# Kernel optimization log

Measured on AMD Instinct MI355X. Metric: run time of the kernel, lower is better.

The kernel has to match this reference:

```python
import jax, jax.numpy as jnp
import numpy as np

B, S, D_IN, D_H = 8, 2048, 512, 512

def setup_inputs() -> dict:
    key = jax.random.key(0)
    ks = jax.random.split(key, 7)
    scale = 1.0 / np.sqrt(D_IN)
    return {
        "x": jax.random.normal(ks[0], (B, S, D_IN), dtype=jnp.float32),
        "Wq": jax.random.uniform(ks[1], (D_IN, D_H), jnp.float32, -scale, scale),
        "bq": jax.random.uniform(ks[2], (D_H,), jnp.float32, -scale, scale),
        "Wk": jax.random.uniform(ks[3], (D_IN, D_H), jnp.float32, -scale, scale),
        "bk": jax.random.uniform(ks[4], (D_H,), jnp.float32, -scale, scale),
        "Wv": jax.random.uniform(ks[5], (D_IN, D_H), jnp.float32, -scale, scale),
        "bv": jax.random.uniform(ks[6], (D_H,), jnp.float32, -scale, scale),
    }

def reference(x, Wq, bq, Wk, bk, Wv, bv):
    q = jnp.einsum("bsd,dh->bsh", x, Wq) + bq  # [B,S,H]
    k = jnp.einsum("bsd,dh->bsh", x, Wk) + bk
    v = jnp.einsum("bsd,dh->bsh", x, Wv) + bv
    # NOTE: original has NO 1/sqrt(d) scaling — faithful reproduction
    scores = jnp.einsum("bqh,bkh->bqk", q, k)  # [B,S,S]
    probs = jax.nn.softmax(scores, axis=-1)
    return jnp.einsum("bqk,bkh->bqh", probs, v)
```

## Files before the change

### kernel.cpp

```cpp
#include <hip/hip_runtime.h>


typedef __attribute__((ext_vector_type(8))) _Float16 f16x8;
typedef __attribute__((ext_vector_type(8))) short bf16x8;
typedef __attribute__((ext_vector_type(4))) float f32x4;

__device__ __forceinline__ unsigned short f2h(float f) {
  _Float16 h = (_Float16)f;
  return *(unsigned short*)&h;
}
__device__ __forceinline__ unsigned short f2bf(float f) {
  unsigned int u = __float_as_uint(f);
  unsigned int r = (u + 0x7fffu + ((u >> 16) & 1u)) >> 16;
  return (unsigned short)r;
}
__device__ __forceinline__ float bf2f(unsigned short h) {
  return __uint_as_float(((unsigned int)h) << 16);
}

__device__ __forceinline__ void load_lds16(const void* g, void* l) {
  __builtin_amdgcn_global_load_lds(
      (const __attribute__((address_space(1))) unsigned int*)g,
      (__attribute__((address_space(3))) unsigned int*)l, 16, 0, 0);
}

__global__ __launch_bounds__(256) void convx_kernel(const float* __restrict__ x,
                                                    unsigned short* __restrict__ xh) {
  int i = blockIdx.x * 256 + threadIdx.x;
  float4 v = ((const float4*)x)[i];
  union { unsigned short h[4]; short4 s4; } u;
  u.h[0] = f2h(v.x); u.h[1] = f2h(v.y); u.h[2] = f2h(v.z); u.h[3] = f2h(v.w);
  ((short4*)xh)[i] = u.s4;
}

__global__ __launch_bounds__(256) void convw_kernel(
    const float* __restrict__ W0, const float* __restrict__ W1,
    const float* __restrict__ W2, unsigned short* __restrict__ Wt) {
  const float* W = (blockIdx.z == 0) ? W0 : (blockIdx.z == 1) ? W1 : W2;
  unsigned short* t = Wt + (size_t)blockIdx.z * 512 * 512;
  __shared__ float tile[32][33];
  int tx = threadIdx.x, ty = threadIdx.y;
  int h0 = blockIdx.x * 32, d0 = blockIdx.y * 32;
  for (int i = ty; i < 32; i += 8) tile[i][tx] = W[(long)(d0 + i) * 512 + h0 + tx];
  __syncthreads();
  for (int i = ty; i < 32; i += 8)
    t[(long)(h0 + i) * 512 + d0 + tx] = f2h(tile[tx][i]);
}

__global__ __launch_bounds__(256) void gemm_qkv_kernel(
    const unsigned short* __restrict__ A,
    const unsigned short* __restrict__ Bt,
    unsigned short* __restrict__ Qo, unsigned short* __restrict__ Ko,
    unsigned short* __restrict__ VTo,
    const float* __restrict__ bq, const float* __restrict__ bk,
    const float* __restrict__ bv) {
  __shared__ alignas(16) unsigned short As[128 * 32];
  __shared__ alignas(16) unsigned short Bs[128 * 32];
  const int t = threadIdx.x;
  const long long bm = (long long)blockIdx.x * 128;
  const long long bn = (long long)blockIdx.y * 128;

  const int ar = t >> 2;
  const int ac = (t & 3) * 8;

  f32x4 acc[4][4];
#pragma unroll
  for (int i = 0; i < 4; i++)
#pragma unroll
    for (int j = 0; j < 4; j++) acc[i][j] = {0.f, 0.f, 0.f, 0.f};

  const int lane = t & 63;
  const int wave = t >> 6;
  const int wm = (wave & 1) * 64;
  const int wn = (wave >> 1) * 64;
  const int fm = lane & 15;
  const int k8 = (lane >> 4) * 8;

  for (int kt = 0; kt < 512; kt += 32) {
#pragma unroll
    for (int r = 0; r < 2; r++)
      load_lds16(A + (bm + r * 64 + ar) * 512 + kt + ac, &As[r * 2048 + t * 8]);
#pragma unroll
    for (int r = 0; r < 2; r++)
      load_lds16(Bt + (bn + r * 64 + ar) * 512 + kt + ac, &Bs[r * 2048 + t * 8]);
    __syncthreads();

    f16x8 af[4], bfr[4];
#pragma unroll
    for (int i = 0; i < 4; i++)
      af[i] = *(const f16x8*)&As[(wm + i * 16 + fm) * 32 + k8];
#pragma unroll
    for (int j = 0; j < 4; j++)
      bfr[j] = *(const f16x8*)&Bs[(wn + j * 16 + fm) * 32 + k8];
#pragma unroll
    for (int i = 0; i < 4; i++)
#pragma unroll
      for (int j = 0; j < 4; j++)
        acc[i][j] = __builtin_amdgcn_mfma_f32_16x16x32_f16(af[i], bfr[j], acc[i][j], 0, 0, 0);
    __syncthreads();
  }

  const int crow = (lane >> 4) * 4;
  const int ccol = lane & 15;
#pragma unroll
  for (int j = 0; j < 4; j++) {
    const long long col = bn + wn + j * 16 + ccol;
    float bias = (col < 512) ? bq[col] : (col < 1024) ? bk[col - 512] : bv[col - 1024];
#pragma unroll
    for (int i = 0; i < 4; i++) {
      const long long row0 = bm + wm + i * 16 + crow;
      if (col >= 1024) {
        const long long b = row0 >> 11;
        const long long s = row0 & 2047;
        const long long dcol = col - 1024;
        union { unsigned short h[4]; short4 s4; } u;
#pragma unroll
        for (int r = 0; r < 4; r++) u.h[r] = f2bf(acc[i][j][r] + bias);
        *(short4*)(VTo + (((b * 64 + (s >> 5)) * 512 + dcol) * 32 + (s & 31))) = u.s4;
      } else {
        unsigned short* dst = (col < 512) ? (Qo + row0 * 512 + col)
                                          : (Ko + row0 * 512 + (col - 512));
#pragma unroll
        for (int r = 0; r < 4; r++) dst[(size_t)r * 512] = f2h(acc[i][j][r] + bias);
      }
    }
  }
}

__global__ __launch_bounds__(512, 2) void attn_fused_kernel(
    const unsigned short* __restrict__ Qg,
    const unsigned short* __restrict__ Kg,
    const unsigned short* __restrict__ Vt,
    float* __restrict__ out) {
  __shared__ alignas(16) unsigned short SB[2][16384];
  __shared__ alignas(16) unsigned short Qh[16384];
  __shared__ alignas(16) unsigned short Ps[8192];
  __shared__ float rsw[4][64];

  const int t = threadIdx.x;
  const int lane = t & 63;
  const int w = t >> 6;
  const int fm = lane & 15;
  const int g = lane >> 4;
  const int qh = w & 1;
  const int kg = w >> 1;
  const int b = blockIdx.x & 7;
  const int q0 = (blockIdx.x >> 3) << 6;

  const unsigned short* Qb = Qg + ((size_t)b * 2048 + q0) * 512;
  const unsigned short* Kb = Kg + (size_t)b * 2048 * 512;
  const unsigned short* Vb = Vt + (size_t)b * 2048 * 512;

  int ksrc[4], qsrc[4]; unsigned int sdst[4];
#pragma unroll
  for (int r = 0; r < 4; ++r) {
    const int L = r * 8192 + t * 16;
    sdst[r] = L >> 1;
    const int kr = L >> 8;
    ksrc[r] = kr * 512 + (((L & 255) ^ ((kr & 7) << 4)) >> 1);
    const int qr = L >> 9;
    qsrc[r] = qr * 512 + (((L & 511) ^ ((qr & 7) << 4)) >> 1);
  }

#pragma unroll
  for (int r = 0; r < 4; ++r) load_lds16(Qb + qsrc[r], &SB[0][sdst[r]]);
#pragma unroll
  for (int r = 0; r < 4; ++r) load_lds16(Qb + 256 + qsrc[r], &Qh[sdst[r]]);
  asm volatile("s_waitcnt vmcnt(4)" ::: "memory");
  __builtin_amdgcn_s_barrier();

  const int swz = (fm & 7) << 4;
  f16x8 qf[2][8];
#pragma unroll
  for (int j = 0; j < 2; ++j)
#pragma unroll
    for (int ds = 0; ds < 8; ++ds)
      qf[j][ds] = *(const f16x8*)((const char*)SB[0] +
          (qh * 32 + j * 16 + fm) * 512 + ((g * 16 + ds * 64) ^ swz));
  asm volatile("s_waitcnt lgkmcnt(0)" ::: "memory");
  __builtin_amdgcn_s_barrier();
#pragma unroll
  for (int r = 0; r < 4; ++r) load_lds16(Kb + ksrc[r], &SB[0][sdst[r]]);

  f32x4 oacc[2][8];
#pragma unroll
  for (int i = 0; i < 2; ++i)
#pragma unroll
    for (int jj = 0; jj < 8; ++jj) oacc[i][jj] = {0.f, 0.f, 0.f, 0.f};
  float psum0 = 0.f, psum1 = 0.f;
  f32x4 sacc[2][2];

  for (int kt = 0; kt < 16; ++kt) {
    const size_t kbase = (size_t)kt * 65536;
#pragma unroll
    for (int u = 0; u < 8; ++u) {
      unsigned short* cur = SB[u & 1];
      unsigned short* nxt = SB[(u & 1) ^ 1];
      if (u < 3) {
#pragma unroll
        for (int r = 0; r < 4; ++r)
          load_lds16(Kb + kbase + (u + 1) * 128 + ksrc[r], &nxt[sdst[r]]);
      } else if (u < 7) {
        const unsigned short* vs = Vb + (size_t)(kt * 4 + (u - 3)) * 16384;
#pragma unroll
        for (int r = 0; r < 4; ++r) load_lds16(vs + sdst[r], &nxt[sdst[r]]);
      } else if (kt < 15) {
#pragma unroll
        for (int r = 0; r < 4; ++r)
          load_lds16(Kb + kbase + 65536 + ksrc[r], &nxt[sdst[r]]);
      }
      if (kt == 15 && u == 7)
        asm volatile("s_waitcnt vmcnt(0)" ::: "memory");
      else
        asm volatile("s_waitcnt vmcnt(4)" ::: "memory");
      __builtin_amdgcn_s_barrier();
      __builtin_amdgcn_sched_barrier(0);

      __builtin_amdgcn_s_setprio(1);
      if (u < 4) {
        if (u == 0) {
          sacc[0][0] = {0.f, 0.f, 0.f, 0.f}; sacc[0][1] = {0.f, 0.f, 0.f, 0.f};
          sacc[1][0] = {0.f, 0.f, 0.f, 0.f}; sacc[1][1] = {0.f, 0.f, 0.f, 0.f};
        }
#pragma unroll
        for (int s = 0; s < 4; ++s) {
          const f16x8 a0 = *(const f16x8*)((const char*)cur +
              (kg * 32 + fm) * 256 + ((g * 16 + s * 64) ^ swz));
          const f16x8 a1 = *(const f16x8*)((const char*)cur +
              (kg * 32 + 16 + fm) * 256 + ((g * 16 + s * 64) ^ swz));
          f16x8 b0, b1;
          if (u < 2) {
            b0 = qf[0][u * 4 + s]; b1 = qf[1][u * 4 + s];
          } else {
            const int dz = (g * 16 + ((u - 2) * 4 + s) * 64) ^ swz;
            b0 = *(const f16x8*)((const char*)Qh + (qh * 32 + fm) * 512 + dz);
            b1 = *(const f16x8*)((const char*)Qh + (qh * 32 + 16 + fm) * 512 + dz);
          }
          sacc[0][0] = __builtin_amdgcn_mfma_f32_16x16x32_f16(a0, b0, sacc[0][0], 0, 0, 0);
          sacc[0][1] = __builtin_amdgcn_mfma_f32_16x16x32_f16(a0, b1, sacc[0][1], 0, 0, 0);
          sacc[1][0] = __builtin_amdgcn_mfma_f32_16x16x32_f16(a1, b0, sacc[1][0], 0, 0, 0);
          sacc[1][1] = __builtin_amdgcn_mfma_f32_16x16x32_f16(a1, b1, sacc[1][1], 0, 0, 0);
        }
        if (u == 3) {
#pragma unroll
          for (int i = 0; i < 2; ++i)
#pragma unroll
            for (int j = 0; j < 2; ++j) {
              const int q = qh * 32 + j * 16 + fm;
              const int k2 = (kg * 32 + i * 16 + g * 4) * 2;
              union { unsigned short h[4]; short4 s4; } uu;
              float s0 = 0.f;
#pragma unroll
              for (int r = 0; r < 4; ++r) {
                const unsigned short pb = f2bf(__expf(sacc[i][j][r]));
                uu.h[r] = pb; s0 += bf2f(pb);
              }
              if (j == 0) psum0 += s0; else psum1 += s0;
              *(short4*)((char*)Ps + q * 256 + (k2 ^ swz)) = uu.s4;
            }
        }
      } else {
        const int ju = u - 4;
        const bf16x8 p0 = *(const bf16x8*)((const char*)Ps +
            (qh * 32 + fm) * 256 + ((ju * 64 + g * 16) ^ swz));
        const bf16x8 p1 = *(const bf16x8*)((const char*)Ps +
            (qh * 32 + 16 + fm) * 256 + ((ju * 64 + g * 16) ^ swz));
#pragma unroll
        for (int jj = 0; jj < 8; ++jj) {
          const bf16x8 vf = *(const bf16x8*)((const char*)cur +
              (kg * 128 + jj * 16 + fm) * 64 + g * 16);
          oacc[0][jj] = __builtin_amdgcn_mfma_f32_16x16x32_bf16(p0, vf, oacc[0][jj], 0, 0, 0);
          oacc[1][jj] = __builtin_amdgcn_mfma_f32_16x16x32_bf16(p1, vf, oacc[1][jj], 0, 0, 0);
        }
      }
      __builtin_amdgcn_s_setprio(0);
      asm volatile("s_waitcnt lgkmcnt(0)" ::: "memory");
      __builtin_amdgcn_s_barrier();
    }
  }

  psum0 += __shfl_xor(psum0, 16); psum0 += __shfl_xor(psum0, 32);
  psum1 += __shfl_xor(psum1, 16); psum1 += __shfl_xor(psum1, 32);
  if (g == 0) {
    rsw[kg][qh * 32 + fm] = psum0;
    rsw[kg][qh * 32 + 16 + fm] = psum1;
  }
  __syncthreads();

  float* ob = out + ((size_t)b * 2048 + q0) * 512;
#pragma unroll
  for (int i = 0; i < 2; ++i) {
    float inv[4];
#pragma unroll
    for (int r = 0; r < 4; ++r) {
      const int q = qh * 32 + i * 16 + g * 4 + r;
      inv[r] = 1.0f / (rsw[0][q] + rsw[1][q] + rsw[2][q] + rsw[3][q]);
    }
#pragma unroll
    for (int jj = 0; jj < 8; ++jj) {
      const int d = kg * 128 + jj * 16 + fm;
#pragma unroll
      for (int r = 0; r < 4; ++r)
        ob[(size_t)(qh * 32 + i * 16 + g * 4 + r) * 512 + d] = oacc[i][jj][r] * inv[r];
    }
  }
}

extern "C" void kernel_launch(void* const* d_in, const int* in_sizes, int n_in,
                              void* d_out, int out_size, void* d_ws, size_t ws_size,
                              hipStream_t stream) {
  const float* x  = (const float*)d_in[0];
  const float* Wq = (const float*)d_in[1];
  const float* bq = (const float*)d_in[2];
  const float* Wk = (const float*)d_in[3];
  const float* bk = (const float*)d_in[4];
  const float* Wv = (const float*)d_in[5];
  const float* bv = (const float*)d_in[6];
  float* out = (float*)d_out;

  const size_t SZ = (size_t)16384 * 512 * 2;
  char* p = (char*)d_ws;
  unsigned short* xh = (unsigned short*)p; p += SZ;
  unsigned short* Wt = (unsigned short*)p; p += (size_t)3 * 512 * 512 * 2;
  unsigned short* Qb = (unsigned short*)p; p += SZ;
  unsigned short* Kb = (unsigned short*)p; p += SZ;
  unsigned short* VT = (unsigned short*)p; p += SZ;

  convx_kernel<<<8192, 256, 0, stream>>>(x, xh);
  convw_kernel<<<dim3(16, 16, 3), dim3(32, 8), 0, stream>>>(Wq, Wk, Wv, Wt);
  gemm_qkv_kernel<<<dim3(128, 12), 256, 0, stream>>>(xh, Wt, Qb, Kb, VT, bq, bk, bv);
  attn_fused_kernel<<<256, 512, 0, stream>>>(Qb, Kb, VT, out);
}
```

Before: 246.6 us.

## Use four-slot LDS ring with two-stage prefetch and keep full Q in registers

After: 301.2 us. 22.1% more time.

```diff
diff --git a/kernel.cpp b/kernel.cpp
--- a/kernel.cpp
+++ b/kernel.cpp
@@ -132,8 +132,7 @@
     const unsigned short* __restrict__ Kg,
     const unsigned short* __restrict__ Vt,
     float* __restrict__ out) {
-  __shared__ alignas(16) unsigned short SB[2][16384];
-  __shared__ alignas(16) unsigned short Qh[16384];
+  __shared__ alignas(16) unsigned short SB[4][16384];
   __shared__ alignas(16) unsigned short Ps[8192];
   __shared__ float rsw[4][64];
 
@@ -158,29 +157,35 @@
     sdst[r] = L >> 1;
     const int kr = L >> 8;
     ksrc[r] = kr * 512 + (((L & 255) ^ ((kr & 7) << 4)) >> 1);
-    const int qr = L >> 9;
-    qsrc[r] = qr * 512 + (((L & 511) ^ ((qr & 7) << 4)) >> 1);
+    const int qr = L >> 10;
+    qsrc[r] = qr * 512 + (((L & 1023) ^ ((qr & 7) << 4)) >> 1);
   }
 
 #pragma unroll
   for (int r = 0; r < 4; ++r) load_lds16(Qb + qsrc[r], &SB[0][sdst[r]]);
 #pragma unroll
-  for (int r = 0; r < 4; ++r) load_lds16(Qb + 256 + qsrc[r], &Qh[sdst[r]]);
-  asm volatile("s_waitcnt vmcnt(4)" ::: "memory");
+  for (int r = 0; r < 4; ++r) load_lds16(Qb + 32 * 512 + qsrc[r], &SB[1][sdst[r]]);
+  asm volatile("s_waitcnt vmcnt(0)" ::: "memory");
   __builtin_amdgcn_s_barrier();
+  __builtin_amdgcn_sched_barrier(0);
 
   const int swz = (fm & 7) << 4;
-  f16x8 qf[2][8];
-#pragma unroll
-  for (int j = 0; j < 2; ++j)
-#pragma unroll
-    for (int ds = 0; ds < 8; ++ds)
-      qf[j][ds] = *(const f16x8*)((const char*)SB[0] +
-          (qh * 32 + j * 16 + fm) * 512 + ((g * 16 + ds * 64) ^ swz));
+  f16x8 qf[2][16];
+#pragma unroll
+  for (int j = 0; j < 2; ++j) {
+    const char* qbase = (const char*)SB[qh] + (j * 16 + fm) * 1024;
+#pragma unroll
+    for (int ds = 0; ds < 16; ++ds)
+      qf[j][ds] = *(const f16x8*)(qbase + ((ds * 64 + g * 16) ^ swz));
+  }
   asm volatile("s_waitcnt lgkmcnt(0)" ::: "memory");
   __builtin_amdgcn_s_barrier();
+  __builtin_amdgcn_sched_barrier(0);
+
 #pragma unroll
   for (int r = 0; r < 4; ++r) load_lds16(Kb + ksrc[r], &SB[0][sdst[r]]);
+#pragma unroll
+  for (int r = 0; r < 4; ++r) load_lds16(Kb + 128 + ksrc[r], &SB[1][sdst[r]]);
 
   f32x4 oacc[2][8];
 #pragma unroll
@@ -194,53 +199,61 @@
     const size_t kbase = (size_t)kt * 65536;
 #pragma unroll
     for (int u = 0; u < 8; ++u) {
-      unsigned short* cur = SB[u & 1];
-      unsigned short* nxt = SB[(u & 1) ^ 1];
-      if (u < 3) {
+      unsigned short* nxt = SB[(u + 2) & 3];
+      if (u == 0) {
 #pragma unroll
         for (int r = 0; r < 4; ++r)
-          load_lds16(Kb + kbase + (u + 1) * 128 + ksrc[r], &nxt[sdst[r]]);
-      } else if (u < 7) {
-        const unsigned short* vs = Vb + (size_t)(kt * 4 + (u - 3)) * 16384;
+          load_lds16(Kb + kbase + 2 * 128 + ksrc[r], &nxt[sdst[r]]);
+      } else if (u == 1) {
+#pragma unroll
+        for (int r = 0; r < 4; ++r)
+          load_lds16(Kb + kbase + 3 * 128 + ksrc[r], &nxt[sdst[r]]);
+      } else if (u < 6) {
+        const unsigned short* vs = Vb + (size_t)(kt * 4 + (u - 2)) * 16384;
 #pragma unroll
         for (int r = 0; r < 4; ++r) load_lds16(vs + sdst[r], &nxt[sdst[r]]);
-      } else if (kt < 15) {
-#pragma unroll
-        for (int r = 0; r < 4; ++r)
-          load_lds16(Kb + kbase + 65536 + ksrc[r], &nxt[sdst[r]]);
+      } else if (u == 6) {
+        if (kt < 15) {
+#pragma unroll
+          for (int r = 0; r < 4; ++r)
+            load_lds16(Kb + kbase + 65536 + ksrc[r], &nxt[sdst[r]]);
+        }
+      } else {
+        if (kt < 15) {
+#pragma unroll
+          for (int r = 0; r < 4; ++r)
+            load_lds16(Kb + kbase + 65536 + 128 + ksrc[r], &nxt[sdst[r]]);
+        }
       }
-      if (kt == 15 && u == 7)
-        asm volatile("s_waitcnt vmcnt(0)" ::: "memory");
-      else
-        asm volatile("s_waitcnt vmcnt(4)" ::: "memory");
+      if (u >= 6 && kt == 15) {
+        if (u == 6) asm volatile("s_waitcnt vmcnt(4)" ::: "memory");
+        else        asm volatile("s_waitcnt vmcnt(0)" ::: "memory");
+      } else {
+        asm volatile("s_waitcnt vmcnt(8)" ::: "memory");
+      }
       __builtin_amdgcn_s_barrier();
       __builtin_amdgcn_sched_barrier(0);
 
-      __builtin_amdgcn_s_setprio(1);
+      const unsigned short* cur = SB[u & 3];
       if (u < 4) {
         if (u == 0) {
           sacc[0][0] = {0.f, 0.f, 0.f, 0.f}; sacc[0][1] = {0.f, 0.f, 0.f, 0.f};
           sacc[1][0] = {0.f, 0.f, 0.f, 0.f}; sacc[1][1] = {0.f, 0.f, 0.f, 0.f};
         }
+        __builtin_amdgcn_s_setprio(1);
 #pragma unroll
         for (int s = 0; s < 4; ++s) {
-          const f16x8 a0 = *(const f16x8*)((const char*)cur +
-              (kg * 32 + fm) * 256 + ((g * 16 + s * 64) ^ swz));
-          const f16x8 a1 = *(const f16x8*)((const char*)cur +
-              (kg * 32 + 16 + fm) * 256 + ((g * 16 + s * 64) ^ swz));
-          f16x8 b0, b1;
-          if (u < 2) {
-            b0 = qf[0][u * 4 + s]; b1 = qf[1][u * 4 + s];
-          } else {
-            const int dz = (g * 16 + ((u - 2) * 4 + s) * 64) ^ swz;
-            b0 = *(const f16x8*)((const char*)Qh + (qh * 32 + fm) * 512 + dz);
-            b1 = *(const f16x8*)((const char*)Qh + (qh * 32 + 16 + fm) * 512 + dz);
-          }
+          const int off = (s * 64 + g * 16) ^ swz;
+          const f16x8 a0 = *(const f16x8*)((const char*)cur + (kg * 32 + fm) * 256 + off);
+          const f16x8 a1 = *(const f16x8*)((const char*)cur + (kg * 32 + 16 + fm) * 256 + off);
+          const f16x8 b0 = qf[0][u * 4 + s];
+          const f16x8 b1 = qf[1][u * 4 + s];
           sacc[0][0] = __builtin_amdgcn_mfma_f32_16x16x32_f16(a0, b0, sacc[0][0], 0, 0, 0);
           sacc[0][1] = __builtin_amdgcn_mfma_f32_16x16x32_f16(a0, b1, sacc[0][1], 0, 0, 0);
           sacc[1][0] = __builtin_amdgcn_mfma_f32_16x16x32_f16(a1, b0, sacc[1][0], 0, 0, 0);
           sacc[1][1] = __builtin_amdgcn_mfma_f32_16x16x32_f16(a1, b1, sacc[1][1], 0, 0, 0);
         }
+        __builtin_amdgcn_s_setprio(0);
         if (u == 3) {
 #pragma unroll
           for (int i = 0; i < 2; ++i)
@@ -258,6 +271,7 @@
               if (j == 0) psum0 += s0; else psum1 += s0;
               *(short4*)((char*)Ps + q * 256 + (k2 ^ swz)) = uu.s4;
             }
+          asm volatile("s_waitcnt lgkmcnt(0)" ::: "memory");
         }
       } else {
         const int ju = u - 4;
@@ -265,6 +279,7 @@
             (qh * 32 + fm) * 256 + ((ju * 64 + g * 16) ^ swz));
         const bf16x8 p1 = *(const bf16x8*)((const char*)Ps +
             (qh * 32 + 16 + fm) * 256 + ((ju * 64 + g * 16) ^ swz));
+        __builtin_amdgcn_s_setprio(1);
 #pragma unroll
         for (int jj = 0; jj < 8; ++jj) {
           const bf16x8 vf = *(const bf16x8*)((const char*)cur +
@@ -272,10 +287,8 @@
           oacc[0][jj] = __builtin_amdgcn_mfma_f32_16x16x32_bf16(p0, vf, oacc[0][jj], 0, 0, 0);
           oacc[1][jj] = __builtin_amdgcn_mfma_f32_16x16x32_bf16(p1, vf, oacc[1][jj], 0, 0, 0);
         }
+        __builtin_amdgcn_s_setprio(0);
       }
-      __builtin_amdgcn_s_setprio(0);
-      asm volatile("s_waitcnt lgkmcnt(0)" ::: "memory");
-      __builtin_amdgcn_s_barrier();
     }
   }
 
```

## Triple-buffer K/V LDS tiles and drop the trailing per-phase barrier

Applied to the files above, without the earlier changes.

New measurement: 329.1 us. 33.4% more time.

```diff
diff --git a/kernel.cpp b/kernel.cpp
--- a/kernel.cpp
+++ b/kernel.cpp
@@ -127,12 +127,123 @@
   }
 }
 
+template <int U>
+__device__ __forceinline__ void qkt_body(const unsigned short* cur, const unsigned short* Qh,
+                                         const f16x8 (&qf)[2][8], f32x4 (&sacc)[2][2],
+                                         int kg, int qh, int fm, int g, int swz) {
+  __builtin_amdgcn_s_setprio(1);
+#pragma unroll
+  for (int s = 0; s < 4; ++s) {
+    const int off = (s * 64 + g * 16) ^ swz;
+    const f16x8 a0 = *(const f16x8*)((const char*)cur + (kg * 32 + fm) * 256 + off);
+    const f16x8 a1 = *(const f16x8*)((const char*)cur + (kg * 32 + 16 + fm) * 256 + off);
+    f16x8 b0, b1;
+    if constexpr (U < 2) {
+      b0 = qf[0][U * 4 + s];
+      b1 = qf[1][U * 4 + s];
+    } else {
+      const int dz = (g * 16 + ((U - 2) * 4 + s) * 64) ^ swz;
+      b0 = *(const f16x8*)((const char*)Qh + (qh * 32 + fm) * 512 + dz);
+      b1 = *(const f16x8*)((const char*)Qh + (qh * 32 + 16 + fm) * 512 + dz);
+    }
+    sacc[0][0] = __builtin_amdgcn_mfma_f32_16x16x32_f16(a0, b0, sacc[0][0], 0, 0, 0);
+    sacc[0][1] = __builtin_amdgcn_mfma_f32_16x16x32_f16(a0, b1, sacc[0][1], 0, 0, 0);
+    sacc[1][0] = __builtin_amdgcn_mfma_f32_16x16x32_f16(a1, b0, sacc[1][0], 0, 0, 0);
+    sacc[1][1] = __builtin_amdgcn_mfma_f32_16x16x32_f16(a1, b1, sacc[1][1], 0, 0, 0);
+  }
+  __builtin_amdgcn_s_setprio(0);
+}
+
+__device__ __forceinline__ void exp_ps(const f32x4 (&sacc)[2][2], unsigned short* Ps,
+                                       float& psum0, float& psum1,
+                                       int kg, int qh, int fm, int g, int swz) {
+#pragma unroll
+  for (int i = 0; i < 2; ++i)
+#pragma unroll
+    for (int j = 0; j < 2; ++j) {
+      const int q = qh * 32 + j * 16 + fm;
+      const int k2 = (kg * 32 + i * 16 + g * 4) * 2;
+      union { unsigned short h[4]; short4 s4; } uu;
+      float s0 = 0.f;
+#pragma unroll
+      for (int r = 0; r < 4; ++r) {
+        const unsigned short pb = f2bf(__expf(sacc[i][j][r]));
+        uu.h[r] = pb; s0 += bf2f(pb);
+      }
+      if (j == 0) psum0 += s0; else psum1 += s0;
+      *(short4*)((char*)Ps + q * 256 + (k2 ^ swz)) = uu.s4;
+    }
+}
+
+template <int JU>
+__device__ __forceinline__ void pv_body(const unsigned short* cur, const unsigned short* Ps,
+                                        f32x4 (&oacc)[2][8],
+                                        int kg, int qh, int fm, int g, int swz) {
+  const bf16x8 p0 = *(const bf16x8*)((const char*)Ps +
+      (qh * 32 + fm) * 256 + ((JU * 64 + g * 16) ^ swz));
+  const bf16x8 p1 = *(const bf16x8*)((const char*)Ps +
+      (qh * 32 + 16 + fm) * 256 + ((JU * 64 + g * 16) ^ swz));
+  __builtin_amdgcn_s_setprio(1);
+#pragma unroll
+  for (int jj = 0; jj < 8; ++jj) {
+    const bf16x8 vf = *(const bf16x8*)((const char*)cur +
+        (kg * 128 + jj * 16 + fm) * 64 + g * 16);
+    oacc[0][jj] = __builtin_amdgcn_mfma_f32_16x16x32_bf16(p0, vf, oacc[0][jj], 0, 0, 0);
+    oacc[1][jj] = __builtin_amdgcn_mfma_f32_16x16x32_bf16(p1, vf, oacc[1][jj], 0, 0, 0);
+  }
+  __builtin_amdgcn_s_setprio(0);
+}
+
+#define PHASE(U, SC, SN, KT, LAST)                                             \
+  do {                                                                         \
+    unsigned short* nx = SB + (SN) * 16384;                                    \
+    if ((U) < 3) {                                                             \
+      const unsigned short* gs = Kb + (size_t)(KT) * 65536 + ((U) + 1) * 128;  \
+      load_lds16(gs + ksrc[0], nx + sdst[0]);                                  \
+      load_lds16(gs + ksrc[1], nx + sdst[1]);                                  \
+      load_lds16(gs + ksrc[2], nx + sdst[2]);                                  \
+      load_lds16(gs + ksrc[3], nx + sdst[3]);                                  \
+    } else if ((U) < 7) {                                                      \
+      const unsigned short* gs = Vb + ((size_t)(KT) * 4 + (U) - 3) * 16384;    \
+      load_lds16(gs + sdst[0], nx + sdst[0]);                                  \
+      load_lds16(gs + sdst[1], nx + sdst[1]);                                  \
+      load_lds16(gs + sdst[2], nx + sdst[2]);                                  \
+      load_lds16(gs + sdst[3], nx + sdst[3]);                                  \
+    } else if (!(LAST)) {                                                      \
+      const unsigned short* gs = Kb + (size_t)((KT) + 1) * 65536;              \
+      load_lds16(gs + ksrc[0], nx + sdst[0]);                                  \
+      load_lds16(gs + ksrc[1], nx + sdst[1]);                                  \
+      load_lds16(gs + ksrc[2], nx + sdst[2]);                                  \
+      load_lds16(gs + ksrc[3], nx + sdst[3]);                                  \
+    }                                                                          \
+    if ((LAST) && (U) == 7) asm volatile("s_waitcnt vmcnt(0)" ::: "memory");   \
+    else                    asm volatile("s_waitcnt vmcnt(4)" ::: "memory");   \
+    __builtin_amdgcn_s_barrier();                                              \
+    __builtin_amdgcn_sched_barrier(0);                                         \
+    {                                                                          \
+      const unsigned short* cur = SB + (SC) * 16384;                           \
+      if ((U) == 0) {                                                          \
+        sacc[0][0] = {0.f, 0.f, 0.f, 0.f}; sacc[0][1] = {0.f, 0.f, 0.f, 0.f}; \
+        sacc[1][0] = {0.f, 0.f, 0.f, 0.f}; sacc[1][1] = {0.f, 0.f, 0.f, 0.f}; \
+      }                                                                        \
+      if ((U) < 4) {                                                           \
+        qkt_body<((U) < 4 ? (U) : 0)>(cur, Qh, qf, sacc, kg, qh, fm, g, swz);  \
+        if ((U) == 3) {                                                        \
+          exp_ps(sacc, Ps, psum0, psum1, kg, qh, fm, g, swz);                  \
+          asm volatile("s_waitcnt lgkmcnt(0)" ::: "memory");                   \
+        }                                                                      \
+      } else {                                                                 \
+        pv_body<((U) >= 4 ? (U) - 4 : 0)>(cur, Ps, oacc, kg, qh, fm, g, swz);  \
+      }                                                                        \
+    }                                                                          \
+  } while (0)
+
 __global__ __launch_bounds__(512, 2) void attn_fused_kernel(
     const unsigned short* __restrict__ Qg,
     const unsigned short* __restrict__ Kg,
     const unsigned short* __restrict__ Vt,
     float* __restrict__ out) {
-  __shared__ alignas(16) unsigned short SB[2][16384];
+  __shared__ alignas(16) unsigned short SB[3 * 16384];
   __shared__ alignas(16) unsigned short Qh[16384];
   __shared__ alignas(16) unsigned short Ps[8192];
   __shared__ float rsw[4][64];
@@ -163,24 +274,28 @@
   }
 
 #pragma unroll
-  for (int r = 0; r < 4; ++r) load_lds16(Qb + qsrc[r], &SB[0][sdst[r]]);
-#pragma unroll
-  for (int r = 0; r < 4; ++r) load_lds16(Qb + 256 + qsrc[r], &Qh[sdst[r]]);
-  asm volatile("s_waitcnt vmcnt(4)" ::: "memory");
+  for (int r = 0; r < 4; ++r) load_lds16(Qb + qsrc[r], SB + sdst[r]);
+#pragma unroll
+  for (int r = 0; r < 4; ++r) load_lds16(Qb + 256 + qsrc[r], Qh + sdst[r]);
+  asm volatile("s_waitcnt vmcnt(0)" ::: "memory");
   __builtin_amdgcn_s_barrier();
+  __builtin_amdgcn_sched_barrier(0);
 
   const int swz = (fm & 7) << 4;
   f16x8 qf[2][8];
 #pragma unroll
-  for (int j = 0; j < 2; ++j)
+  for (int j = 0; j < 2; ++j) {
+    const char* qbase = (const char*)SB + (qh * 32 + j * 16 + fm) * 512;
 #pragma unroll
     for (int ds = 0; ds < 8; ++ds)
-      qf[j][ds] = *(const f16x8*)((const char*)SB[0] +
-          (qh * 32 + j * 16 + fm) * 512 + ((g * 16 + ds * 64) ^ swz));
+      qf[j][ds] = *(const f16x8*)(qbase + ((g * 16 + ds * 64) ^ swz));
+  }
   asm volatile("s_waitcnt lgkmcnt(0)" ::: "memory");
   __builtin_amdgcn_s_barrier();
-#pragma unroll
-  for (int r = 0; r < 4; ++r) load_lds16(Kb + ksrc[r], &SB[0][sdst[r]]);
+  __builtin_amdgcn_sched_barrier(0);
+
+#pragma unroll
+  for (int r = 0; r < 4; ++r) load_lds16(Kb + ksrc[r], SB + sdst[r]);
 
   f32x4 oacc[2][8];
 #pragma unroll
@@ -190,94 +305,17 @@
   float psum0 = 0.f, psum1 = 0.f;
   f32x4 sacc[2][2];
 
-  for (int kt = 0; kt < 16; ++kt) {
-    const size_t kbase = (size_t)kt * 65536;
-#pragma unroll
-    for (int u = 0; u < 8; ++u) {
-      unsigned short* cur = SB[u & 1];
-      unsigned short* nxt = SB[(u & 1) ^ 1];
-      if (u < 3) {
-#pragma unroll
-        for (int r = 0; r < 4; ++r)
-          load_lds16(Kb + kbase + (u + 1) * 128 + ksrc[r], &nxt[sdst[r]]);
-      } else if (u < 7) {
-        const unsigned short* vs = Vb + (size_t)(kt * 4 + (u - 3)) * 16384;
-#pragma unroll
-        for (int r = 0; r < 4; ++r) load_lds16(vs + sdst[r], &nxt[sdst[r]]);
-      } else if (kt < 15) {
-#pragma unroll
-        for (int r = 0; r < 4; ++r)
-          load_lds16(Kb + kbase + 65536 + ksrc[r], &nxt[sdst[r]]);
-      }
-      if (kt == 15 && u == 7)
-        asm volatile("s_waitcnt vmcnt(0)" ::: "memory");
-      else
-        asm volatile("s_waitcnt vmcnt(4)" ::: "memory");
-      __builtin_amdgcn_s_barrier();
-      __builtin_amdgcn_sched_barrier(0);
-
-      __builtin_amdgcn_s_setprio(1);
-      if (u < 4) {
-        if (u == 0) {
-          sacc[0][0] = {0.f, 0.f, 0.f, 0.f}; sacc[0][1] = {0.f, 0.f, 0.f, 0.f};
-          sacc[1][0] = {0.f, 0.f, 0.f, 0.f}; sacc[1][1] = {0.f, 0.f, 0.f, 0.f};
-        }
-#pragma unroll
-        for (int s = 0; s < 4; ++s) {
-          const f16x8 a0 = *(const f16x8*)((const char*)cur +
-              (kg * 32 + fm) * 256 + ((g * 16 + s * 64) ^ swz));
-          const f16x8 a1 = *(const f16x8*)((const char*)cur +
-              (kg * 32 + 16 + fm) * 256 + ((g * 16 + s * 64) ^ swz));
-          f16x8 b0, b1;
-          if (u < 2) {
-            b0 = qf[0][u * 4 + s]; b1 = qf[1][u * 4 + s];
-          } else {
-            const int dz = (g * 16 + ((u - 2) * 4 + s) * 64) ^ swz;
-            b0 = *(const f16x8*)((const char*)Qh + (qh * 32 + fm) * 512 + dz);
-            b1 = *(const f16x8*)((const char*)Qh + (qh * 32 + 16 + fm) * 512 + dz);
-          }
-          sacc[0][0] = __builtin_amdgcn_mfma_f32_16x16x32_f16(a0, b0, sacc[0][0], 0, 0, 0);
-          sacc[0][1] = __builtin_amdgcn_mfma_f32_16x16x32_f16(a0, b1, sacc[0][1], 0, 0, 0);
-          sacc[1][0] = __builtin_amdgcn_mfma_f32_16x16x32_f16(a1, b0, sacc[1][0], 0, 0, 0);
-          sacc[1][1] = __builtin_amdgcn_mfma_f32_16x16x32_f16(a1, b1, sacc[1][1], 0, 0, 0);
-        }
-        if (u == 3) {
-#pragma unroll
-          for (int i = 0; i < 2; ++i)
-#pragma unroll
-            for (int j = 0; j < 2; ++j) {
-              const int q = qh * 32 + j * 16 + fm;
-              const int k2 = (kg * 32 + i * 16 + g * 4) * 2;
-              union { unsigned short h[4]; short4 s4; } uu;
-              float s0 = 0.f;
-#pragma unroll
-              for (int r = 0; r < 4; ++r) {
-                const unsigned short pb = f2bf(__expf(sacc[i][j][r]));
-                uu.h[r] = pb; s0 += bf2f(pb);
-              }
-              if (j == 0) psum0 += s0; else psum1 += s0;
-              *(short4*)((char*)Ps + q * 256 + (k2 ^ swz)) = uu.s4;
-            }
-        }
-      } else {
-        const int ju = u - 4;
-        const bf16x8 p0 = *(const bf16x8*)((const char*)Ps +
-            (qh * 32 + fm) * 256 + ((ju * 64 + g * 16) ^ swz));
-        const bf16x8 p1 = *(const bf16x8*)((const char*)Ps +
-            (qh * 32 + 16 + fm) * 256 + ((ju * 64 + g * 16) ^ swz));
-#pragma unroll
-        for (int jj = 0; jj < 8; ++jj) {
-          const bf16x8 vf = *(const bf16x8*)((const char*)cur +
-              (kg * 128 + jj * 16 + fm) * 64 + g * 16);
-          oacc[0][jj] = __builtin_amdgcn_mfma_f32_16x16x32_bf16(p0, vf, oacc[0][jj], 0, 0, 0);
-          oacc[1][jj] = __builtin_amdgcn_mfma_f32_16x16x32_bf16(p1, vf, oacc[1][jj], 0, 0, 0);
-        }
-      }
-      __builtin_amdgcn_s_setprio(0);
-      asm volatile("s_waitcnt lgkmcnt(0)" ::: "memory");
-      __builtin_amdgcn_s_barrier();
-    }
-  }
+  for (int m = 0; m < 5; ++m) {
+    const int k0 = 3 * m;
+    PHASE(0, 0, 1, k0, 0); PHASE(1, 1, 2, k0, 0); PHASE(2, 2, 0, k0, 0); PHASE(3, 0, 1, k0, 0);
+    PHASE(4, 1, 2, k0, 0); PHASE(5, 2, 0, k0, 0); PHASE(6, 0, 1, k0, 0); PHASE(7, 1, 2, k0, 0);
+    PHASE(0, 2, 0, k0 + 1, 0); PHASE(1, 0, 1, k0 + 1, 0); PHASE(2, 1, 2, k0 + 1, 0); PHASE(3, 2, 0, k0 + 1, 0);
+    PHASE(4, 0, 1, k0 + 1, 0); PHASE(5, 1, 2, k0 + 1, 0); PHASE(6, 2, 0, k0 + 1, 0); PHASE(7, 0, 1, k0 + 1, 0);
+    PHASE(0, 1, 2, k0 + 2, 0); PHASE(1, 2, 0, k0 + 2, 0); PHASE(2, 0, 1, k0 + 2, 0); PHASE(3, 1, 2, k0 + 2, 0);
+    PHASE(4, 2, 0, k0 + 2, 0); PHASE(5, 0, 1, k0 + 2, 0); PHASE(6, 1, 2, k0 + 2, 0); PHASE(7, 2, 0, k0 + 2, 0);
+  }
+  PHASE(0, 0, 1, 15, 0); PHASE(1, 1, 2, 15, 0); PHASE(2, 2, 0, 15, 0); PHASE(3, 0, 1, 15, 0);
+  PHASE(4, 1, 2, 15, 0); PHASE(5, 2, 0, 15, 0); PHASE(6, 0, 1, 15, 0); PHASE(7, 1, 2, 15, 1);
 
   psum0 += __shfl_xor(psum0, 16); psum0 += __shfl_xor(psum0, 32);
   psum1 += __shfl_xor(psum1, 16); psum1 += __shfl_xor(psum1, 32);
```
